# Performance work log

Hardware: AMD Instinct MI355X
Metric: run time of the kernel (lower is better)

Reference implementation:

```python
import jax, jax.numpy as jnp
import numpy as np


def setup_inputs() -> dict:
    key = jax.random.key(0)
    k1, k2 = jax.random.split(key)
    set1 = jax.random.normal(k1, (8192, 256), dtype=jnp.float32)
    set2 = jax.random.normal(k2, (8192, 256), dtype=jnp.float32)
    return {"set1": set1, "set2": set2}


def reference(set1, set2):
    # Pairwise Euclidean distances via the Gram trick:
    sq1 = jnp.sum(set1 * set1, axis=-1)  # [N]
    sq2 = jnp.sum(set2 * set2, axis=-1)  # [M]
    gram = jnp.einsum('nd,md->nm', set1, set2)  # [N,M]
    d2 = sq1[:, None] + sq2[None, :] - 2.0 * gram
    d = jnp.sqrt(jnp.maximum(d2, 0.0))  # clamp tiny negatives from roundoff
    term_1 = jnp.mean(jnp.min(d, axis=1))  # for each point in set1, nearest in set2
    term_2 = jnp.mean(jnp.min(d, axis=0))  # for each point in set2, nearest in set1
    return term_1 + term_2
```

## Files before the change

kernel.cpp:

```cpp
#include <hip/hip_runtime.h>

#define N_PTS 8192
#define D_DIM 256
#define BN 256
#define BM 128
#define BK 64
#define INF_BITS 0x7F800000u

typedef __attribute__((ext_vector_type(8))) short short8;
typedef __attribute__((ext_vector_type(4))) float f32x4;

__device__ __forceinline__ void gload_lds16(const ushort* g, ushort* l) {
    __builtin_amdgcn_global_load_lds(
        (const __attribute__((address_space(1))) void*)g,
        (__attribute__((address_space(3))) void*)l, 16, 0, 0);
}

__device__ __forceinline__ ushort f2bf(float x) {
    unsigned u = __float_as_uint(x);
    return (ushort)((u + 0x7FFFu + ((u >> 16) & 1u)) >> 16);
}

__global__ void prep_kernel(const float* __restrict__ s1, const float* __restrict__ s2,
                            ushort* __restrict__ b1, ushort* __restrict__ b2,
                            float* __restrict__ sq1, float* __restrict__ sq2,
                            unsigned* __restrict__ rowmin2, unsigned* __restrict__ colmin2) {
    const int half = N_PTS * D_DIM;
    int t = blockIdx.x * 256 + threadIdx.x;
    int e = t * 8;
    bool first = e < half;
    const float* src = first ? s1 : s2;
    ushort* dst = first ? b1 : b2;
    int off = first ? e : e - half;
    float4 v0 = *(const float4*)(src + off);
    float4 v1 = *(const float4*)(src + off + 4);
    float s = v0.x * v0.x + v0.y * v0.y + v0.z * v0.z + v0.w * v0.w
            + v1.x * v1.x + v1.y * v1.y + v1.z * v1.z + v1.w * v1.w;
    ushort4 o0 = { f2bf(v0.x), f2bf(v0.y), f2bf(v0.z), f2bf(v0.w) };
    ushort4 o1 = { f2bf(v1.x), f2bf(v1.y), f2bf(v1.z), f2bf(v1.w) };
    *(ushort4*)(dst + off)     = o0;
    *(ushort4*)(dst + off + 4) = o1;
    #pragma unroll
    for (int m = 1; m <= 16; m <<= 1) s += __shfl_xor(s, m, 64);
    int sub = threadIdx.x & 31;
    int row = off >> 8;
    if (sub == 0) (first ? sq1 : sq2)[row] = s;
    if (sub == 1) (first ? rowmin2 : colmin2)[row] = INF_BITS;
}

__global__ __launch_bounds__(256, 2) void tile_kernel(
    const ushort* __restrict__ B1, const ushort* __restrict__ B2,
    const float* __restrict__ sq1, const float* __restrict__ sq2,
    unsigned* __restrict__ rowmin2, unsigned* __restrict__ colmin2) {
    __shared__ ushort As[BN * BK] __attribute__((aligned(16)));
    __shared__ ushort Bs[BM * BK] __attribute__((aligned(16)));
    __shared__ unsigned rs[BN];
    __shared__ unsigned cs[BM];

    const int tid  = threadIdx.x;
    const int lane = tid & 63;
    const int w    = tid >> 6;
    const int quad = lane >> 4;
    const int c    = lane & 15;
    const int n_off = (w >> 1) * 128;
    const int m_off = (w & 1) * 64;
    const int n0 = blockIdx.y * BN;
    const int m0 = blockIdx.x * BM;

    rs[tid] = INF_BITS;
    if (tid < BM) cs[tid] = INF_BITS;

    f32x4 acc[8][4];
    #pragma unroll
    for (int ti = 0; ti < 8; ti++)
        #pragma unroll
        for (int tj = 0; tj < 4; tj++) acc[ti][tj] = (f32x4){0.f, 0.f, 0.f, 0.f};

    for (int k0 = 0; k0 < D_DIM; k0 += BK) {
        #pragma unroll
        for (int r = 0; r < 8; r++) {
            int idx = r * 256 + tid;
            int row = idx >> 3;
            int gc  = (idx & 7) ^ (row & 7);
            gload_lds16(B1 + (size_t)(n0 + row) * D_DIM + k0 + gc * 8,
                        &As[(idx & ~63) * 8]);
        }
        #pragma unroll
        for (int r = 0; r < 4; r++) {
            int idx = r * 256 + tid;
            int row = idx >> 3;
            int gc  = (idx & 7) ^ (row & 7);
            gload_lds16(B2 + (size_t)(m0 + row) * D_DIM + k0 + gc * 8,
                        &Bs[(idx & ~63) * 8]);
        }
        __syncthreads();

        #pragma unroll
        for (int kk = 0; kk < 2; kk++) {
            short8 a[8], b[4];
            #pragma unroll
            for (int ti = 0; ti < 8; ti++) {
                int row = n_off + ti * 16 + c;
                int ch  = (kk * 4 + quad) ^ (row & 7);
                a[ti] = *(const short8*)&As[row * BK + ch * 8];
            }
            #pragma unroll
            for (int tj = 0; tj < 4; tj++) {
                int row = m_off + tj * 16 + c;
                int ch  = (kk * 4 + quad) ^ (row & 7);
                b[tj] = *(const short8*)&Bs[row * BK + ch * 8];
            }
            #pragma unroll
            for (int ti = 0; ti < 8; ti++)
                #pragma unroll
                for (int tj = 0; tj < 4; tj++)
                    acc[ti][tj] = __builtin_amdgcn_mfma_f32_16x16x32_bf16(
                        a[ti], b[tj], acc[ti][tj], 0, 0, 0);
        }
        __syncthreads();
    }

    float sqm[4];
    #pragma unroll
    for (int tj = 0; tj < 4; tj++) sqm[tj] = sq2[m0 + m_off + tj * 16 + c];
    float cmin[4];
    #pragma unroll
    for (int tj = 0; tj < 4; tj++) cmin[tj] = __uint_as_float(INF_BITS);

    #pragma unroll
    for (int ti = 0; ti < 8; ti++) {
        float4 sqn = *(const float4*)&sq1[n0 + n_off + ti * 16 + quad * 4];
        float rmin[4] = { __uint_as_float(INF_BITS), __uint_as_float(INF_BITS),
                          __uint_as_float(INF_BITS), __uint_as_float(INF_BITS) };
        #pragma unroll
        for (int tj = 0; tj < 4; tj++) {
            float sn[4] = { sqn.x, sqn.y, sqn.z, sqn.w };
            #pragma unroll
            for (int r = 0; r < 4; r++) {
                float d2 = fmaxf(sn[r] + sqm[tj] - 2.f * acc[ti][tj][r], 0.f);
                rmin[r]  = fminf(rmin[r], d2);
                cmin[tj] = fminf(cmin[tj], d2);
            }
        }
        #pragma unroll
        for (int m = 1; m <= 8; m <<= 1)
            #pragma unroll
            for (int r = 0; r < 4; r++)
                rmin[r] = fminf(rmin[r], __shfl_xor(rmin[r], m, 64));
        if (c == 0) {
            #pragma unroll
            for (int r = 0; r < 4; r++)
                atomicMin(&rs[n_off + ti * 16 + quad * 4 + r], __float_as_uint(rmin[r]));
        }
    }
    #pragma unroll
    for (int m = 16; m <= 32; m <<= 1)
        #pragma unroll
        for (int tj = 0; tj < 4; tj++)
            cmin[tj] = fminf(cmin[tj], __shfl_xor(cmin[tj], m, 64));
    if (quad == 0) {
        #pragma unroll
        for (int tj = 0; tj < 4; tj++)
            atomicMin(&cs[m_off + tj * 16 + c], __float_as_uint(cmin[tj]));
    }
    __syncthreads();

    atomicMin(&rowmin2[n0 + tid], rs[tid]);
    if (tid < BM) atomicMin(&colmin2[m0 + tid], cs[tid]);
}

__global__ __launch_bounds__(1024) void reduce_kernel(const unsigned* __restrict__ mins,
                                                      float* __restrict__ out) {
    int tid = threadIdx.x;
    uint4 v[4];
    #pragma unroll
    for (int j = 0; j < 4; j++) v[j] = ((const uint4*)mins)[j * 1024 + tid];
    float s = 0.f;
    #pragma unroll
    for (int j = 0; j < 4; j++)
        s += sqrtf(__uint_as_float(v[j].x)) + sqrtf(__uint_as_float(v[j].y))
           + sqrtf(__uint_as_float(v[j].z)) + sqrtf(__uint_as_float(v[j].w));
    #pragma unroll
    for (int m = 32; m > 0; m >>= 1) s += __shfl_xor(s, m, 64);
    __shared__ float ws[16];
    int lane = tid & 63, wv = tid >> 6;
    if (lane == 0) ws[wv] = s;
    __syncthreads();
    if (tid < 16) {
        float t = ws[tid];
        #pragma unroll
        for (int m = 8; m > 0; m >>= 1) t += __shfl_xor(t, m, 64);
        if (tid == 0) out[0] = t / (float)N_PTS;
    }
}

extern "C" void kernel_launch(void* const* d_in, const int* in_sizes, int n_in,
                              void* d_out, int out_size, void* d_ws, size_t ws_size,
                              hipStream_t stream) {
    const float* set1 = (const float*)d_in[0];
    const float* set2 = (const float*)d_in[1];
    float* out = (float*)d_out;

    unsigned* rowmin2 = (unsigned*)d_ws;
    unsigned* colmin2 = rowmin2 + N_PTS;
    float* sq1 = (float*)(colmin2 + N_PTS);
    float* sq2 = sq1 + N_PTS;
    ushort* b1 = (ushort*)((char*)d_ws + 128 * 1024);
    ushort* b2 = b1 + (size_t)N_PTS * D_DIM;

    prep_kernel<<<(2 * N_PTS * D_DIM) / (256 * 8), 256, 0, stream>>>(
        set1, set2, b1, b2, sq1, sq2, rowmin2, colmin2);
    tile_kernel<<<dim3(N_PTS / BM, N_PTS / BN), 256, 0, stream>>>(
        b1, b2, sq1, sq2, rowmin2, colmin2);
    reduce_kernel<<<1, 1024, 0, stream>>>(rowmin2, out);
}
```

Baseline: 118.5 us.

## Enlarge tile to 256x256 with 512 threads and double-buffered LDS prefetch

Grows the output tile to 256x256 and the block to 512 threads (8 waves), which halves the number of blocks and reduces redundant B1 loads. The K loop now double-buffers A/B tiles in LDS and issues the next stage's global-to-LDS loads while the current MFMAs run, using explicit barriers, waitcnts and setprio around the MFMA bursts. The cost is more LDS per block (64KB of staging), which may limit occupancy, and only 1024 blocks to spread across the CUs.

```diff
diff --git a/kernel.cpp b/kernel.cpp
--- a/kernel.cpp
+++ b/kernel.cpp
@@ -3,7 +3,7 @@
 #define N_PTS 8192
 #define D_DIM 256
 #define BN 256
-#define BM 128
+#define BM 256
 #define BK 64
 #define INF_BITS 0x7F800000u
 
@@ -48,12 +48,22 @@
     if (sub == 1) (first ? rowmin2 : colmin2)[row] = INF_BITS;
 }
 
-__global__ __launch_bounds__(256, 2) void tile_kernel(
+__device__ __forceinline__ void stage256(const ushort* __restrict__ g, ushort* l, int tid) {
+    #pragma unroll
+    for (int r = 0; r < 4; r++) {
+        int idx = r * 512 + tid;
+        int row = idx >> 3;
+        int gc  = (idx & 7) ^ (row & 7);
+        gload_lds16(g + (size_t)row * D_DIM + gc * 8, &l[(idx & ~63) * 8]);
+    }
+}
+
+__global__ __launch_bounds__(512, 2) void tile_kernel(
     const ushort* __restrict__ B1, const ushort* __restrict__ B2,
     const float* __restrict__ sq1, const float* __restrict__ sq2,
     unsigned* __restrict__ rowmin2, unsigned* __restrict__ colmin2) {
-    __shared__ ushort As[BN * BK] __attribute__((aligned(16)));
-    __shared__ ushort Bs[BM * BK] __attribute__((aligned(16)));
+    __shared__ ushort As[2][BN * BK] __attribute__((aligned(16)));
+    __shared__ ushort Bs[2][BM * BK] __attribute__((aligned(16)));
     __shared__ unsigned rs[BN];
     __shared__ unsigned cs[BM];
 
@@ -62,13 +72,13 @@
     const int w    = tid >> 6;
     const int quad = lane >> 4;
     const int c    = lane & 15;
-    const int n_off = (w >> 1) * 128;
-    const int m_off = (w & 1) * 64;
+    const int n_off = (w >> 2) * 128;
+    const int m_off = (w & 3) * 64;
     const int n0 = blockIdx.y * BN;
     const int m0 = blockIdx.x * BM;
 
-    rs[tid] = INF_BITS;
-    if (tid < BM) cs[tid] = INF_BITS;
+    if (tid < BN) rs[tid] = INF_BITS;
+    else          cs[tid - BN] = INF_BITS;
 
     f32x4 acc[8][4];
     #pragma unroll
@@ -76,48 +86,51 @@
         #pragma unroll
         for (int tj = 0; tj < 4; tj++) acc[ti][tj] = (f32x4){0.f, 0.f, 0.f, 0.f};
 
-    for (int k0 = 0; k0 < D_DIM; k0 += BK) {
-        #pragma unroll
-        for (int r = 0; r < 8; r++) {
-            int idx = r * 256 + tid;
-            int row = idx >> 3;
-            int gc  = (idx & 7) ^ (row & 7);
-            gload_lds16(B1 + (size_t)(n0 + row) * D_DIM + k0 + gc * 8,
-                        &As[(idx & ~63) * 8]);
+    const ushort* gA = B1 + (size_t)n0 * D_DIM;
+    const ushort* gB = B2 + (size_t)m0 * D_DIM;
+
+    stage256(gA, As[0], tid);
+    stage256(gB, Bs[0], tid);
+    asm volatile("s_waitcnt vmcnt(0)" ::: "memory");
+    __builtin_amdgcn_s_barrier();
+
+    #pragma unroll 4
+    for (int t = 0; t < 4; ++t) {
+        const ushort* cA = As[t & 1];
+        const ushort* cB = Bs[t & 1];
+        #pragma unroll
+        for (int p = 0; p < 4; ++p) {
+            const int kk = p >> 1;
+            const int h  = p & 1;
+            short8 a[4], b[4];
+            #pragma unroll
+            for (int i = 0; i < 4; i++) {
+                int row = n_off + (h * 4 + i) * 16 + c;
+                int ch  = (kk * 4 + quad) ^ (row & 7);
+                a[i] = *(const short8*)&cA[row * BK + ch * 8];
+            }
+            #pragma unroll
+            for (int j = 0; j < 4; j++) {
+                int row = m_off + j * 16 + c;
+                int ch  = (kk * 4 + quad) ^ (row & 7);
+                b[j] = *(const short8*)&cB[row * BK + ch * 8];
+            }
+            if (t < 3 && p == 0) stage256(gA + (t + 1) * BK, As[(t + 1) & 1], tid);
+            if (t < 3 && p == 1) stage256(gB + (t + 1) * BK, Bs[(t + 1) & 1], tid);
+
+            __builtin_amdgcn_s_barrier();
+            asm volatile("s_waitcnt lgkmcnt(0)" ::: "memory");
+            __builtin_amdgcn_s_setprio(1);
+            #pragma unroll
+            for (int i = 0; i < 4; i++)
+                #pragma unroll
+                for (int j = 0; j < 4; j++)
+                    acc[h * 4 + i][j] = __builtin_amdgcn_mfma_f32_16x16x32_bf16(
+                        a[i], b[j], acc[h * 4 + i][j], 0, 0, 0);
+            __builtin_amdgcn_s_setprio(0);
+            if (p == 3 && t < 3) asm volatile("s_waitcnt vmcnt(0)" ::: "memory");
+            __builtin_amdgcn_s_barrier();
         }
-        #pragma unroll
-        for (int r = 0; r < 4; r++) {
-            int idx = r * 256 + tid;
-            int row = idx >> 3;
-            int gc  = (idx & 7) ^ (row & 7);
-            gload_lds16(B2 + (size_t)(m0 + row) * D_DIM + k0 + gc * 8,
-                        &Bs[(idx & ~63) * 8]);
-        }
-        __syncthreads();
-
-        #pragma unroll
-        for (int kk = 0; kk < 2; kk++) {
-            short8 a[8], b[4];
-            #pragma unroll
-            for (int ti = 0; ti < 8; ti++) {
-                int row = n_off + ti * 16 + c;
-                int ch  = (kk * 4 + quad) ^ (row & 7);
-                a[ti] = *(const short8*)&As[row * BK + ch * 8];
-            }
-            #pragma unroll
-            for (int tj = 0; tj < 4; tj++) {
-                int row = m_off + tj * 16 + c;
-                int ch  = (kk * 4 + quad) ^ (row & 7);
-                b[tj] = *(const short8*)&Bs[row * BK + ch * 8];
-            }
-            #pragma unroll
-            for (int ti = 0; ti < 8; ti++)
-                #pragma unroll
-                for (int tj = 0; tj < 4; tj++)
-                    acc[ti][tj] = __builtin_amdgcn_mfma_f32_16x16x32_bf16(
-                        a[ti], b[tj], acc[ti][tj], 0, 0, 0);
-        }
-        __syncthreads();
     }
 
     float sqm[4];
@@ -165,8 +178,8 @@
     }
     __syncthreads();
 
-    atomicMin(&rowmin2[n0 + tid], rs[tid]);
-    if (tid < BM) atomicMin(&colmin2[m0 + tid], cs[tid]);
+    if (tid < BN) atomicMin(&rowmin2[n0 + tid], rs[tid]);
+    else          atomicMin(&colmin2[m0 + tid - BN], cs[tid - BN]);
 }
 
 __global__ __launch_bounds__(1024) void reduce_kernel(const unsigned* __restrict__ mins,
@@ -210,7 +223,7 @@
 
     prep_kernel<<<(2 * N_PTS * D_DIM) / (256 * 8), 256, 0, stream>>>(
         set1, set2, b1, b2, sq1, sq2, rowmin2, colmin2);
-    tile_kernel<<<dim3(N_PTS / BM, N_PTS / BN), 256, 0, stream>>>(
+    tile_kernel<<<dim3(N_PTS / BM, N_PTS / BN), 512, 0, stream>>>(
         b1, b2, sq1, sq2, rowmin2, colmin2);
     reduce_kernel<<<1, 1024, 0, stream>>>(rowmin2, out);
 }
```

New measurement: 122.3 us. 3.2% more time.

## Double-buffer LDS tiles with BK=32 to overlap global loads with MFMA

Applied to the files above, without the earlier changes.

Halves the K-tile to 32 and allocates two LDS buffers for A and B. The next tile is prefetched via global_load_lds while MFMAs run on the current one, with a new XOR swizzle suited to 4 chunks per row. The aim is to hide global-load latency that the single-buffered loop exposed at each sync. In exchange there are twice as many iterations and barriers, and the prefetch may not be waited on correctly, since global_load_lds completion depends on vmcnt being drained before the barrier.

```diff
diff --git a/kernel.cpp b/kernel.cpp
--- a/kernel.cpp
+++ b/kernel.cpp
@@ -4,7 +4,7 @@
 #define D_DIM 256
 #define BN 256
 #define BM 128
-#define BK 64
+#define BK 32
 #define INF_BITS 0x7F800000u
 
 typedef __attribute__((ext_vector_type(8))) short short8;
@@ -48,12 +48,31 @@
     if (sub == 1) (first ? rowmin2 : colmin2)[row] = INF_BITS;
 }
 
+__device__ __forceinline__ void stageA(const ushort* __restrict__ g, ushort* l, int tid) {
+    #pragma unroll
+    for (int r = 0; r < 4; r++) {
+        int idx = r * 256 + tid;
+        int row = idx >> 2;
+        int gc  = (idx & 3) ^ ((row >> 1) & 3);
+        gload_lds16(g + (size_t)row * D_DIM + gc * 8, &l[(idx & ~63) * 8]);
+    }
+}
+__device__ __forceinline__ void stageB(const ushort* __restrict__ g, ushort* l, int tid) {
+    #pragma unroll
+    for (int r = 0; r < 2; r++) {
+        int idx = r * 256 + tid;
+        int row = idx >> 2;
+        int gc  = (idx & 3) ^ ((row >> 1) & 3);
+        gload_lds16(g + (size_t)row * D_DIM + gc * 8, &l[(idx & ~63) * 8]);
+    }
+}
+
 __global__ __launch_bounds__(256, 2) void tile_kernel(
     const ushort* __restrict__ B1, const ushort* __restrict__ B2,
     const float* __restrict__ sq1, const float* __restrict__ sq2,
     unsigned* __restrict__ rowmin2, unsigned* __restrict__ colmin2) {
-    __shared__ ushort As[BN * BK] __attribute__((aligned(16)));
-    __shared__ ushort Bs[BM * BK] __attribute__((aligned(16)));
+    __shared__ ushort As[2][BN * BK] __attribute__((aligned(16)));
+    __shared__ ushort Bs[2][BM * BK] __attribute__((aligned(16)));
     __shared__ unsigned rs[BN];
     __shared__ unsigned cs[BM];
 
@@ -76,47 +95,40 @@
         #pragma unroll
         for (int tj = 0; tj < 4; tj++) acc[ti][tj] = (f32x4){0.f, 0.f, 0.f, 0.f};
 
-    for (int k0 = 0; k0 < D_DIM; k0 += BK) {
-        #pragma unroll
-        for (int r = 0; r < 8; r++) {
-            int idx = r * 256 + tid;
-            int row = idx >> 3;
-            int gc  = (idx & 7) ^ (row & 7);
-            gload_lds16(B1 + (size_t)(n0 + row) * D_DIM + k0 + gc * 8,
-                        &As[(idx & ~63) * 8]);
-        }
-        #pragma unroll
-        for (int r = 0; r < 4; r++) {
-            int idx = r * 256 + tid;
-            int row = idx >> 3;
-            int gc  = (idx & 7) ^ (row & 7);
-            gload_lds16(B2 + (size_t)(m0 + row) * D_DIM + k0 + gc * 8,
-                        &Bs[(idx & ~63) * 8]);
-        }
-        __syncthreads();
-
-        #pragma unroll
-        for (int kk = 0; kk < 2; kk++) {
-            short8 a[8], b[4];
-            #pragma unroll
-            for (int ti = 0; ti < 8; ti++) {
-                int row = n_off + ti * 16 + c;
-                int ch  = (kk * 4 + quad) ^ (row & 7);
-                a[ti] = *(const short8*)&As[row * BK + ch * 8];
-            }
-            #pragma unroll
-            for (int tj = 0; tj < 4; tj++) {
-                int row = m_off + tj * 16 + c;
-                int ch  = (kk * 4 + quad) ^ (row & 7);
-                b[tj] = *(const short8*)&Bs[row * BK + ch * 8];
-            }
-            #pragma unroll
-            for (int ti = 0; ti < 8; ti++)
-                #pragma unroll
-                for (int tj = 0; tj < 4; tj++)
-                    acc[ti][tj] = __builtin_amdgcn_mfma_f32_16x16x32_bf16(
-                        a[ti], b[tj], acc[ti][tj], 0, 0, 0);
-        }
+    const ushort* gA = B1 + (size_t)n0 * D_DIM;
+    const ushort* gB = B2 + (size_t)m0 * D_DIM;
+
+    stageA(gA, As[0], tid);
+    stageB(gB, Bs[0], tid);
+    __syncthreads();
+
+    #pragma unroll
+    for (int t = 0; t < D_DIM / BK; ++t) {
+        if (t < D_DIM / BK - 1) {
+            stageA(gA + (t + 1) * BK, As[(t + 1) & 1], tid);
+            stageB(gB + (t + 1) * BK, Bs[(t + 1) & 1], tid);
+        }
+        const ushort* cA = As[t & 1];
+        const ushort* cB = Bs[t & 1];
+        short8 a[8], b[4];
+        #pragma unroll
+        for (int j = 0; j < 4; j++) {
+            int row = m_off + j * 16 + c;
+            int sc  = quad ^ ((row >> 1) & 3);
+            b[j] = *(const short8*)&cB[row * BK + sc * 8];
+        }
+        #pragma unroll
+        for (int i = 0; i < 8; i++) {
+            int row = n_off + i * 16 + c;
+            int sc  = quad ^ ((row >> 1) & 3);
+            a[i] = *(const short8*)&cA[row * BK + sc * 8];
+        }
+        #pragma unroll
+        for (int i = 0; i < 8; i++)
+            #pragma unroll
+            for (int j = 0; j < 4; j++)
+                acc[i][j] = __builtin_amdgcn_mfma_f32_16x16x32_bf16(
+                    a[i], b[j], acc[i][j], 0, 0, 0);
         __syncthreads();
     }
 
```

Measured after the change: 123.6 us. 4.3% more time.

## Switch to 32x32x16 MFMA with k-major LDS layout and fuse final reduction

Applied to the files above, without the earlier changes.

Replaces the 16x16x32 bf16 MFMA tiling with 32x32x16 MFMAs and restructures the LDS layout so each global_load_lds writes a contiguous k-slab that lanes read directly without XOR swizzling. The epilogue is reworked to the 32x32 accumulator layout, with per-column minima reduced by shuffles. The separate reduce kernel is removed: the last block to finish, detected through a global atomic counter, sums the square roots of the minima. This aims to cut LDS read instructions per MFMA and one kernel launch, at the cost of a larger register array for column minima and a serialized tail in one block.

```diff
diff --git a/kernel.cpp b/kernel.cpp
--- a/kernel.cpp
+++ b/kernel.cpp
@@ -8,7 +8,9 @@
 #define INF_BITS 0x7F800000u
 
 typedef __attribute__((ext_vector_type(8))) short short8;
-typedef __attribute__((ext_vector_type(4))) float f32x4;
+typedef __attribute__((ext_vector_type(16))) float f32x16;
+
+__device__ unsigned g_cnt;
 
 __device__ __forceinline__ void gload_lds16(const ushort* g, ushort* l) {
     __builtin_amdgcn_global_load_lds(
@@ -27,6 +29,7 @@
                             unsigned* __restrict__ rowmin2, unsigned* __restrict__ colmin2) {
     const int half = N_PTS * D_DIM;
     int t = blockIdx.x * 256 + threadIdx.x;
+    if (t == 0) atomicExch(&g_cnt, 0u);
     int e = t * 8;
     bool first = e < half;
     const float* src = first ? s1 : s2;
@@ -51,17 +54,20 @@
 __global__ __launch_bounds__(256, 2) void tile_kernel(
     const ushort* __restrict__ B1, const ushort* __restrict__ B2,
     const float* __restrict__ sq1, const float* __restrict__ sq2,
-    unsigned* __restrict__ rowmin2, unsigned* __restrict__ colmin2) {
+    unsigned* __restrict__ rowmin2, unsigned* __restrict__ colmin2,
+    float* __restrict__ out) {
     __shared__ ushort As[BN * BK] __attribute__((aligned(16)));
     __shared__ ushort Bs[BM * BK] __attribute__((aligned(16)));
     __shared__ unsigned rs[BN];
     __shared__ unsigned cs[BM];
+    __shared__ float wsum[4];
+    __shared__ unsigned lastf;
 
     const int tid  = threadIdx.x;
     const int lane = tid & 63;
     const int w    = tid >> 6;
-    const int quad = lane >> 4;
-    const int c    = lane & 15;
+    const int hi   = lane >> 5;
+    const int l31  = lane & 31;
     const int n_off = (w >> 1) * 128;
     const int m_off = (w & 1) * 64;
     const int n0 = blockIdx.y * BN;
@@ -70,127 +76,112 @@
     rs[tid] = INF_BITS;
     if (tid < BM) cs[tid] = INF_BITS;
 
-    f32x4 acc[8][4];
-    #pragma unroll
-    for (int ti = 0; ti < 8; ti++)
-        #pragma unroll
-        for (int tj = 0; tj < 4; tj++) acc[ti][tj] = (f32x4){0.f, 0.f, 0.f, 0.f};
-
-    for (int k0 = 0; k0 < D_DIM; k0 += BK) {
-        #pragma unroll
-        for (int r = 0; r < 8; r++) {
-            int idx = r * 256 + tid;
-            int row = idx >> 3;
-            int gc  = (idx & 7) ^ (row & 7);
-            gload_lds16(B1 + (size_t)(n0 + row) * D_DIM + k0 + gc * 8,
-                        &As[(idx & ~63) * 8]);
-        }
-        #pragma unroll
-        for (int r = 0; r < 4; r++) {
-            int idx = r * 256 + tid;
-            int row = idx >> 3;
-            int gc  = (idx & 7) ^ (row & 7);
-            gload_lds16(B2 + (size_t)(m0 + row) * D_DIM + k0 + gc * 8,
-                        &Bs[(idx & ~63) * 8]);
+    f32x16 acc[2][4];
+    #pragma unroll
+    for (int fm = 0; fm < 2; fm++)
+        #pragma unroll
+        for (int fn = 0; fn < 4; fn++)
+            acc[fm][fn] = (f32x16){0.f,0.f,0.f,0.f,0.f,0.f,0.f,0.f,
+                                   0.f,0.f,0.f,0.f,0.f,0.f,0.f,0.f};
+
+    const ushort* gA = B1 + (size_t)(n0 + l31) * D_DIM + w * 16 + hi * 8;
+    const ushort* gB = B2 + (size_t)(m0 + l31) * D_DIM + w * 16 + hi * 8;
+
+    #pragma unroll
+    for (int t = 0; t < D_DIM / BK; ++t) {
+        #pragma unroll
+        for (int r = 0; r < 8; r++)
+            gload_lds16(gA + t * BK + r * 32 * D_DIM, &As[(r * 256 + w * 64) * 8]);
+        #pragma unroll
+        for (int r = 0; r < 4; r++)
+            gload_lds16(gB + t * BK + r * 32 * D_DIM, &Bs[(r * 256 + w * 64) * 8]);
+        __syncthreads();
+
+        #pragma unroll
+        for (int ks = 0; ks < 4; ks++) {
+            short8 av[2], bv[4];
+            #pragma unroll
+            for (int fm = 0; fm < 2; fm++)
+                av[fm] = *(const short8*)&Bs[(((w & 1) * 2 + fm) * 4 + ks) * 512 + lane * 8];
+            #pragma unroll
+            for (int fn = 0; fn < 4; fn++)
+                bv[fn] = *(const short8*)&As[(((w >> 1) * 4 + fn) * 4 + ks) * 512 + lane * 8];
+            #pragma unroll
+            for (int fm = 0; fm < 2; fm++)
+                #pragma unroll
+                for (int fn = 0; fn < 4; fn++)
+                    acc[fm][fn] = __builtin_amdgcn_mfma_f32_32x32x16_bf16(
+                        av[fm], bv[fn], acc[fm][fn], 0, 0, 0);
         }
         __syncthreads();
-
-        #pragma unroll
-        for (int kk = 0; kk < 2; kk++) {
-            short8 a[8], b[4];
-            #pragma unroll
-            for (int ti = 0; ti < 8; ti++) {
-                int row = n_off + ti * 16 + c;
-                int ch  = (kk * 4 + quad) ^ (row & 7);
-                a[ti] = *(const short8*)&As[row * BK + ch * 8];
-            }
-            #pragma unroll
-            for (int tj = 0; tj < 4; tj++) {
-                int row = m_off + tj * 16 + c;
-                int ch  = (kk * 4 + quad) ^ (row & 7);
-                b[tj] = *(const short8*)&Bs[row * BK + ch * 8];
-            }
-            #pragma unroll
-            for (int ti = 0; ti < 8; ti++)
+    }
+
+    float sq1v[4];
+    #pragma unroll
+    for (int fn = 0; fn < 4; fn++) sq1v[fn] = sq1[n0 + n_off + fn * 32 + l31];
+    float rmin[4];
+    #pragma unroll
+    for (int fn = 0; fn < 4; fn++) rmin[fn] = __uint_as_float(INF_BITS);
+    float cmn[32];
+
+    #pragma unroll
+    for (int fm = 0; fm < 2; fm++) {
+        #pragma unroll
+        for (int q = 0; q < 4; q++) {
+            float4 s2 = *(const float4*)&sq2[m0 + m_off + fm * 32 + hi * 4 + q * 8];
+            float s2a[4] = { s2.x, s2.y, s2.z, s2.w };
+            #pragma unroll
+            for (int rr = 0; rr < 4; rr++) {
+                const int r = q * 4 + rr;
+                float cm = __uint_as_float(INF_BITS);
                 #pragma unroll
-                for (int tj = 0; tj < 4; tj++)
-                    acc[ti][tj] = __builtin_amdgcn_mfma_f32_16x16x32_bf16(
-                        a[ti], b[tj], acc[ti][tj], 0, 0, 0);
-        }
-        __syncthreads();
-    }
-
-    float sqm[4];
-    #pragma unroll
-    for (int tj = 0; tj < 4; tj++) sqm[tj] = sq2[m0 + m_off + tj * 16 + c];
-    float cmin[4];
-    #pragma unroll
-    for (int tj = 0; tj < 4; tj++) cmin[tj] = __uint_as_float(INF_BITS);
-
-    #pragma unroll
-    for (int ti = 0; ti < 8; ti++) {
-        float4 sqn = *(const float4*)&sq1[n0 + n_off + ti * 16 + quad * 4];
-        float rmin[4] = { __uint_as_float(INF_BITS), __uint_as_float(INF_BITS),
-                          __uint_as_float(INF_BITS), __uint_as_float(INF_BITS) };
-        #pragma unroll
-        for (int tj = 0; tj < 4; tj++) {
-            float sn[4] = { sqn.x, sqn.y, sqn.z, sqn.w };
-            #pragma unroll
-            for (int r = 0; r < 4; r++) {
-                float d2 = fmaxf(sn[r] + sqm[tj] - 2.f * acc[ti][tj][r], 0.f);
-                rmin[r]  = fminf(rmin[r], d2);
-                cmin[tj] = fminf(cmin[tj], d2);
+                for (int fn = 0; fn < 4; fn++) {
+                    float d2 = fmaxf(fmaf(-2.f, acc[fm][fn][r], sq1v[fn] + s2a[rr]), 0.f);
+                    rmin[fn] = fminf(rmin[fn], d2);
+                    cm = fminf(cm, d2);
+                }
+                cmn[fm * 16 + r] = cm;
             }
         }
-        #pragma unroll
-        for (int m = 1; m <= 8; m <<= 1)
-            #pragma unroll
-            for (int r = 0; r < 4; r++)
-                rmin[r] = fminf(rmin[r], __shfl_xor(rmin[r], m, 64));
-        if (c == 0) {
-            #pragma unroll
-            for (int r = 0; r < 4; r++)
-                atomicMin(&rs[n_off + ti * 16 + quad * 4 + r], __float_as_uint(rmin[r]));
-        }
-    }
-    #pragma unroll
-    for (int m = 16; m <= 32; m <<= 1)
-        #pragma unroll
-        for (int tj = 0; tj < 4; tj++)
-            cmin[tj] = fminf(cmin[tj], __shfl_xor(cmin[tj], m, 64));
-    if (quad == 0) {
-        #pragma unroll
-        for (int tj = 0; tj < 4; tj++)
-            atomicMin(&cs[m_off + tj * 16 + c], __float_as_uint(cmin[tj]));
+    }
+    #pragma unroll
+    for (int fn = 0; fn < 4; fn++)
+        atomicMin(&rs[n_off + fn * 32 + l31], __float_as_uint(rmin[fn]));
+    #pragma unroll
+    for (int m = 1; m <= 16; m <<= 1)
+        #pragma unroll
+        for (int i = 0; i < 32; i++)
+            cmn[i] = fminf(cmn[i], __shfl_xor(cmn[i], m, 64));
+    if (l31 == 0) {
+        #pragma unroll
+        for (int fm = 0; fm < 2; fm++)
+            #pragma unroll
+            for (int r = 0; r < 16; r++)
+                atomicMin(&cs[m_off + fm * 32 + (r & 3) + (r >> 2) * 8 + hi * 4],
+                          __float_as_uint(cmn[fm * 16 + r]));
     }
     __syncthreads();
 
     atomicMin(&rowmin2[n0 + tid], rs[tid]);
     if (tid < BM) atomicMin(&colmin2[m0 + tid], cs[tid]);
-}
-
-__global__ __launch_bounds__(1024) void reduce_kernel(const unsigned* __restrict__ mins,
-                                                      float* __restrict__ out) {
-    int tid = threadIdx.x;
-    uint4 v[4];
-    #pragma unroll
-    for (int j = 0; j < 4; j++) v[j] = ((const uint4*)mins)[j * 1024 + tid];
-    float s = 0.f;
-    #pragma unroll
-    for (int j = 0; j < 4; j++)
-        s += sqrtf(__uint_as_float(v[j].x)) + sqrtf(__uint_as_float(v[j].y))
-           + sqrtf(__uint_as_float(v[j].z)) + sqrtf(__uint_as_float(v[j].w));
-    #pragma unroll
-    for (int m = 32; m > 0; m >>= 1) s += __shfl_xor(s, m, 64);
-    __shared__ float ws[16];
-    int lane = tid & 63, wv = tid >> 6;
-    if (lane == 0) ws[wv] = s;
+
+    __threadfence();
+    if (tid == 0)
+        lastf = (atomicAdd(&g_cnt, 1u) == (unsigned)(gridDim.x * gridDim.y - 1));
     __syncthreads();
-    if (tid < 16) {
-        float t = ws[tid];
-        #pragma unroll
-        for (int m = 8; m > 0; m >>= 1) t += __shfl_xor(t, m, 64);
-        if (tid == 0) out[0] = t / (float)N_PTS;
+    if (lastf) {
+        float s = 0.f;
+        #pragma unroll 8
+        for (int j = 0; j < 64; ++j) {
+            unsigned u = __hip_atomic_load(&rowmin2[tid + 256 * j],
+                                           __ATOMIC_RELAXED, __HIP_MEMORY_SCOPE_AGENT);
+            s += sqrtf(__uint_as_float(u));
+        }
+        #pragma unroll
+        for (int m = 1; m <= 32; m <<= 1) s += __shfl_xor(s, m, 64);
+        if (lane == 0) wsum[w] = s;
+        __syncthreads();
+        if (tid == 0) out[0] = (wsum[0] + wsum[1] + wsum[2] + wsum[3]) / (float)N_PTS;
     }
 }
 
@@ -211,6 +202,5 @@
     prep_kernel<<<(2 * N_PTS * D_DIM) / (256 * 8), 256, 0, stream>>>(
         set1, set2, b1, b2, sq1, sq2, rowmin2, colmin2);
     tile_kernel<<<dim3(N_PTS / BM, N_PTS / BN), 256, 0, stream>>>(
-        b1, b2, sq1, sq2, rowmin2, colmin2);
-    reduce_kernel<<<1, 1024, 0, stream>>>(rowmin2, out);
-}
+        b1, b2, sq1, sq2, rowmin2, colmin2, out);
+}
```

After: 246.8 us. 108% more time.
